# Kernel tuning notes

Measured on AMD Instinct MI355X. Metric: run time of the kernel, lower is better.

The kernel has to match this reference:

```python
import jax, jax.numpy as jnp
import numpy as np

EMBED_DIM = 1024
B, S = 8, 4096

def setup_inputs() -> dict:
    key = jax.random.key(0)
    k_x, k_w1, k_b1, k_phi, k_w2, k_b2 = jax.random.split(key, 6)
    lim1 = 1.0 / np.sqrt(EMBED_DIM)
    lim2 = 1.0  # linear2 fan_in = ffn_dim = 1
    return {
        "x": jax.random.normal(k_x, (B, S, EMBED_DIM), dtype=jnp.float32),
        "W1": jax.random.uniform(k_w1, (1, EMBED_DIM), jnp.float32, -lim1, lim1),
        "b1": jax.random.uniform(k_b1, (1,), jnp.float32, -lim1, lim1),
        "phi": jax.random.uniform(k_phi, (), jnp.float32, 0.0, 2.0 * np.pi),
        "W2": jax.random.uniform(k_w2, (EMBED_DIM, 1), jnp.float32, -lim2, lim2),
        "b2": jax.random.uniform(k_b2, (EMBED_DIM,), jnp.float32, -lim2, lim2),
    }

def reference(x, W1, b1, phi, W2, b2):
    # linear1: per-token projection to a scalar angle theta  [B,S,1]
    theta = jnp.einsum("bsd,od->bso", x, W1) + b1
    # 1-qubit circuit RY(theta) -> RX(phi) -> <PauliZ> on |0>
    # closed form: <Z> = cos(theta) * cos(phi)
    q = jnp.cos(theta) * jnp.cos(phi)  # [B,S,1]
    # dropout=0 (eval); linear2: ffn_dim(=1) -> embed_dim
    out = jnp.einsum("bso,do->bsd", q, W2) + b2  # [B,S,EMBED_DIM]
    return out
```

## Files before the change

kernel.cpp:

```cpp
#include <hip/hip_runtime.h>
#include <math.h>


#define EMBED_D 1024
#define NTOK    (8 * 4096)

typedef float f4 __attribute__((ext_vector_type(4)));

__global__ __launch_bounds__(256) void ffq_theta(
    const float* __restrict__ x,
    const float* __restrict__ W1,
    const float* __restrict__ b1,
    const float* __restrict__ phi,
    float* __restrict__ q_ws)
{
    const int lane = threadIdx.x & 63;
    const int wib  = threadIdx.x >> 6;
    const int tok  = blockIdx.x * 4 + wib;

    const f4* x4 = (const f4*)x + (size_t)tok * (EMBED_D / 4);
    f4 xv[4];
    #pragma unroll
    for (int c = 0; c < 4; ++c) xv[c] = x4[c * 64 + lane];

    const f4* w14 = (const f4*)W1;
    f4 w1r[4];
    #pragma unroll
    for (int c = 0; c < 4; ++c) w1r[c] = w14[c * 64 + lane];

    float s = 0.f;
    #pragma unroll
    for (int c = 0; c < 4; ++c) {
        s = fmaf(xv[c].x, w1r[c].x, s);
        s = fmaf(xv[c].y, w1r[c].y, s);
        s = fmaf(xv[c].z, w1r[c].z, s);
        s = fmaf(xv[c].w, w1r[c].w, s);
    }

    #pragma unroll
    for (int m = 32; m > 0; m >>= 1)
        s += __shfl_xor(s, m, 64);

    if (lane == 0)
        q_ws[tok] = cosf(s + b1[0]) * cosf(phi[0]);
}

__global__ __launch_bounds__(256) void ffq_out(
    const float* __restrict__ q_ws,
    const float* __restrict__ W2,
    const float* __restrict__ b2,
    float* __restrict__ out)
{
    const int t = threadIdx.x;
    const int b = blockIdx.x;

    const f4 qv  = ((const f4*)q_ws)[b];
    const f4 w2v = ((const f4*)W2)[t];
    const f4 b2v = ((const f4*)b2)[t];

    f4* ob = (f4*)out + (size_t)b * 4 * (EMBED_D / 4);
    const float qq[4] = { qv.x, qv.y, qv.z, qv.w };

    #pragma unroll
    for (int tt = 0; tt < 4; ++tt) {
        f4 o;
        o.x = fmaf(qq[tt], w2v.x, b2v.x);
        o.y = fmaf(qq[tt], w2v.y, b2v.y);
        o.z = fmaf(qq[tt], w2v.z, b2v.z);
        o.w = fmaf(qq[tt], w2v.w, b2v.w);
        __builtin_nontemporal_store(o, &ob[tt * (EMBED_D / 4) + t]);
    }
}

extern "C" void kernel_launch(void* const* d_in, const int* in_sizes, int n_in,
                              void* d_out, int out_size, void* d_ws, size_t ws_size,
                              hipStream_t stream) {
    const float* x   = (const float*)d_in[0];
    const float* W1  = (const float*)d_in[1];
    const float* b1  = (const float*)d_in[2];
    const float* phi = (const float*)d_in[3];
    const float* W2  = (const float*)d_in[4];
    const float* b2  = (const float*)d_in[5];
    float* out = (float*)d_out;
    float* q_ws = (float*)d_ws;

    ffq_theta<<<NTOK / 4, 256, 0, stream>>>(x, W1, b1, phi, q_ws);
    ffq_out<<<NTOK / 4, 256, 0, stream>>>(q_ws, W2, b2, out);
}
```

Baseline: 236.2 us.

## Split theta dot into partial-sum and reduce kernels; widen output tiles

The token dot product is split into two kernels. The first kernel has each wave process four rows and write 64 per-lane partial sums to workspace, without the cross-lane shuffle reduction. A second kernel reduces those partials in groups of 16 lanes and applies the cosine. The output kernel now handles 16 tokens per block and switches from nontemporal to plain stores. This adds an extra launch and about 8 MB of partial-sum traffic through workspace, in exchange for fewer shuffles and less per-block overhead.

Result: slower. 249.8 us (+5.7%).

```diff
diff --git a/kernel.cpp b/kernel.cpp
--- a/kernel.cpp
+++ b/kernel.cpp
@@ -3,46 +3,59 @@
 
 
 #define EMBED_D 1024
+#define ROW_F4  (EMBED_D / 4)
 #define NTOK    (8 * 4096)
+#define P1_BLOCKS 2048
+#define P1_PASSES 4
+#define TPB3    16
 
 typedef float f4 __attribute__((ext_vector_type(4)));
 
-__global__ __launch_bounds__(256) void ffq_theta(
+__global__ __launch_bounds__(256) void ffq_partial(
     const float* __restrict__ x,
     const float* __restrict__ W1,
-    const float* __restrict__ b1,
-    const float* __restrict__ phi,
-    float* __restrict__ q_ws)
+    float* __restrict__ part)
 {
     const int lane = threadIdx.x & 63;
-    const int wib  = threadIdx.x >> 6;
-    const int tok  = blockIdx.x * 4 + wib;
-
-    const f4* x4 = (const f4*)x + (size_t)tok * (EMBED_D / 4);
-    f4 xv[4];
-    #pragma unroll
-    for (int c = 0; c < 4; ++c) xv[c] = x4[c * 64 + lane];
+    const int wid  = blockIdx.x * 4 + (threadIdx.x >> 6);
 
     const f4* w14 = (const f4*)W1;
     f4 w1r[4];
     #pragma unroll
     for (int c = 0; c < 4; ++c) w1r[c] = w14[c * 64 + lane];
 
-    float s = 0.f;
     #pragma unroll
-    for (int c = 0; c < 4; ++c) {
-        s = fmaf(xv[c].x, w1r[c].x, s);
-        s = fmaf(xv[c].y, w1r[c].y, s);
-        s = fmaf(xv[c].z, w1r[c].z, s);
-        s = fmaf(xv[c].w, w1r[c].w, s);
+    for (int p = 0; p < P1_PASSES; ++p) {
+        const int row = p * 8192 + wid;
+        const f4* xr = (const f4*)x + (size_t)row * ROW_F4;
+        f4 x0 = xr[0 * 64 + lane];
+        f4 x1 = xr[1 * 64 + lane];
+        f4 x2 = xr[2 * 64 + lane];
+        f4 x3 = xr[3 * 64 + lane];
+        f4 a = x0 * w1r[0];
+        a += x1 * w1r[1];
+        a += x2 * w1r[2];
+        a += x3 * w1r[3];
+        part[(size_t)row * 64 + lane] = a.x + a.y + a.z + a.w;
     }
+}
 
-    #pragma unroll
-    for (int m = 32; m > 0; m >>= 1)
-        s += __shfl_xor(s, m, 64);
-
-    if (lane == 0)
-        q_ws[tok] = cosf(s + b1[0]) * cosf(phi[0]);
+__global__ __launch_bounds__(256) void ffq_reduce(
+    const float* __restrict__ part,
+    const float* __restrict__ b1,
+    const float* __restrict__ phi,
+    float* __restrict__ q)
+{
+    const int t = threadIdx.x;
+    const int g = blockIdx.x * 256 + t;
+    const f4 v = ((const f4*)part)[g];
+    float s = (v.x + v.y) + (v.z + v.w);
+    s += __shfl_xor(s, 1, 16);
+    s += __shfl_xor(s, 2, 16);
+    s += __shfl_xor(s, 4, 16);
+    s += __shfl_xor(s, 8, 16);
+    if ((t & 15) == 0)
+        q[g >> 4] = cosf(s + b1[0]) * cosf(phi[0]);
 }
 
 __global__ __launch_bounds__(256) void ffq_out(
@@ -52,23 +65,24 @@
     float* __restrict__ out)
 {
     const int t = threadIdx.x;
-    const int b = blockIdx.x;
 
-    const f4 qv  = ((const f4*)q_ws)[b];
     const f4 w2v = ((const f4*)W2)[t];
     const f4 b2v = ((const f4*)b2)[t];
 
-    f4* ob = (f4*)out + (size_t)b * 4 * (EMBED_D / 4);
-    const float qq[4] = { qv.x, qv.y, qv.z, qv.w };
+    const f4* qb = (const f4*)q_ws + blockIdx.x * (TPB3 / 4);
+    f4 q0 = qb[0], q1 = qb[1], q2 = qb[2], q3 = qb[3];
+    const float qq[TPB3] = { q0.x,q0.y,q0.z,q0.w, q1.x,q1.y,q1.z,q1.w,
+                             q2.x,q2.y,q2.z,q2.w, q3.x,q3.y,q3.z,q3.w };
 
+    f4* ob = (f4*)out + (size_t)blockIdx.x * TPB3 * ROW_F4 + t;
     #pragma unroll
-    for (int tt = 0; tt < 4; ++tt) {
+    for (int tt = 0; tt < TPB3; ++tt) {
         f4 o;
         o.x = fmaf(qq[tt], w2v.x, b2v.x);
         o.y = fmaf(qq[tt], w2v.y, b2v.y);
         o.z = fmaf(qq[tt], w2v.z, b2v.z);
         o.w = fmaf(qq[tt], w2v.w, b2v.w);
-        __builtin_nontemporal_store(o, &ob[tt * (EMBED_D / 4) + t]);
+        ob[tt * ROW_F4] = o;
     }
 }
 
@@ -82,8 +96,11 @@
     const float* W2  = (const float*)d_in[4];
     const float* b2  = (const float*)d_in[5];
     float* out = (float*)d_out;
-    float* q_ws = (float*)d_ws;
 
-    ffq_theta<<<NTOK / 4, 256, 0, stream>>>(x, W1, b1, phi, q_ws);
-    ffq_out<<<NTOK / 4, 256, 0, stream>>>(q_ws, W2, b2, out);
+    float* part = (float*)d_ws;
+    float* q    = (float*)d_ws + (size_t)NTOK * 64;
+
+    ffq_partial<<<P1_BLOCKS, 256, 0, stream>>>(x, W1, part);
+    ffq_reduce <<<NTOK * 16 / 256, 256, 0, stream>>>(part, b1, phi, q);
+    ffq_out    <<<NTOK / TPB3, 256, 0, stream>>>(q, W2, b2, out);
 }
```
